# Kernel tuning notes

Measured on AMD Instinct MI355X. Metric: run time of the kernel, lower is better.

The kernel has to match this reference:

```python
import jax, jax.numpy as jnp
import numpy as np

B, S, E = 8, 2048, 8   # batch, seq, embed_dim (embed_dim forced to 8 by module structure)
NQ = 8                 # n_qubits
FF = 4096              # ffn_dim
LN_EPS = 1e-5


def setup_inputs() -> dict:
    key = jax.random.key(0)
    ks = jax.random.split(key, 16)
    rn = lambda k, shape, s=1.0: jax.random.normal(k, shape, dtype=jnp.float32) * s
    return {
        "x": rn(ks[0], (B, S, E)),
        "w_pre": rn(ks[1], (E, NQ), 0.3), "b_pre": rn(ks[2], (NQ,), 0.1),
        "th_q": rn(ks[3], (NQ,)), "th_k": rn(ks[4], (NQ,)), "th_v": rn(ks[5], (NQ,)),
        "w_comb": rn(ks[6], (E, E), 0.3), "b_comb": rn(ks[7], (E,), 0.1),
        "g1": jnp.ones((E,), jnp.float32), "be1": jnp.zeros((E,), jnp.float32),
        "g2": jnp.ones((E,), jnp.float32), "be2": jnp.zeros((E,), jnp.float32),
        "w_pre_f": rn(ks[8], (E, NQ), 0.3), "b_pre_f": rn(ks[9], (NQ,), 0.1),
        "th_f": rn(ks[10], (NQ,)),
        "w1": rn(ks[11], (NQ, FF), 0.3), "b1": rn(ks[12], (FF,), 0.1),
        "w2": rn(ks[13], (FF, E), 0.02), "b2": rn(ks[14], (E,), 0.1),
    }


def _qproj(z, theta):
    # Exact closed form of: RX(z_i)RX(theta_i) per wire on |0>, CNOT chain
    # (0,1)...(6,7),(7,0), then <Z_w>. CNOTs permute basis states; for the
    # resulting product distribution: <Z_k> = prod_{i<=k} cos(phi_i) (k>=1),
    # <Z_0> = prod_{i=1..NQ-1} cos(phi_i), with phi = z + theta.
    c = jnp.cos(z + theta)                 # [N, NQ]
    cp = jnp.cumprod(c, axis=-1)           # out_k for k>=1
    out0 = jnp.prod(c[..., 1:], axis=-1)   # wire 0
    return cp.at[..., 0].set(out0)


def _layernorm(z, g, b):
    m = jnp.mean(z, axis=-1, keepdims=True)
    v = jnp.var(z, axis=-1, keepdims=True)
    return (z - m) * jax.lax.rsqrt(v + LN_EPS) * g + b


def reference(x, w_pre, b_pre, th_q, th_k, th_v, w_comb, b_comb,
              g1, be1, g2, be2, w_pre_f, b_pre_f, th_f, w1, b1, w2, b2):
    b, s, e = x.shape
    xf = x.reshape(b * s, e)
    qin = xf @ w_pre + b_pre                       # shared pre_proj for q/k/v
    Q = _qproj(qin, th_q).reshape(b, s, e)         # num_heads=1, d_k=e=8
    K = _qproj(qin, th_k).reshape(b, s, e)
    V = _qproj(qin, th_v).reshape(b, s, e)
    scores = jnp.einsum('bqd,bkd->bqk', Q, K) / jnp.sqrt(jnp.float32(e))
    probs = jax.nn.softmax(scores, axis=-1)        # dropout=0 (eval)
    attn = jnp.einsum('bqk,bkd->bqd', probs, V)
    attn_out = attn @ w_comb + b_comb
    h = _layernorm(x + attn_out, g1, be1)
    hf = h.reshape(b * s, e)
    qf = _qproj(hf @ w_pre_f + b_pre_f, th_f)
    ff = jax.nn.relu(qf @ w1 + b1) @ w2 + b2
    return _layernorm(h + ff.reshape(b, s, e), g2, be2)
```

## Files before the change

kernel.cpp:

```cpp
#include <hip/hip_runtime.h>
#include <hip/hip_bf16.h>

#define BB 8
#define SS 2048
#define EE 8
#define FF 4096
#define NTOK (BB*SS)

using bf16x8 = __attribute__((ext_vector_type(8))) short;
using f32x4  = __attribute__((ext_vector_type(4))) float;

constexpr int O_FLAG  = 0;
constexpr int O_WPRE  = 8;
constexpr int O_BPRE  = 72;
constexpr int O_THQ   = 80;
constexpr int O_THK   = 88;
constexpr int O_THV   = 96;
constexpr int O_WCOMB = 104;
constexpr int O_BCOMB = 168;
constexpr int O_G1    = 176;
constexpr int O_BE1   = 184;
constexpr int O_G2    = 192;
constexpr int O_BE2   = 200;
constexpr int O_WPREF = 208;
constexpr int O_BPREF = 272;
constexpr int O_THF   = 280;
constexpr int O_B2    = 288;
constexpr int O_W1T   = 512;
constexpr int O_B1F   = O_W1T + FF*8;
constexpr int O_W2F   = O_B1F + FF;
constexpr int O_X     = O_W2F + FF*8;
constexpr int O_K     = O_X + NTOK*EE;
constexpr int O_V     = O_K + NTOK*EE;
constexpr int O_H     = O_V + NTOK*EE;
constexpr int O_P     = O_H + NTOK*EE;
constexpr int O_QFB   = O_P + 8*NTOK*EE;
constexpr int O_W1A   = O_QFB + NTOK*4;
constexpr int O_W2B   = O_W1A + 65536;
constexpr int O_QB    = O_W2B + 32768;
constexpr int O_KB    = O_QB + NTOK*4;
constexpr int O_VTB   = O_KB + NTOK*4;
constexpr size_t WS_MFMA = (size_t)(O_VTB + 65536) * 4;

__device__ __forceinline__ float b2f(unsigned short u) {
  return __uint_as_float(((unsigned)u) << 16);
}

__device__ __forceinline__ unsigned short f2bf(float f) {
  unsigned u = __float_as_uint(f);
  unsigned r = (u + 0x7fffu + ((u >> 16) & 1u)) >> 16;
  return (unsigned short)r;
}

__device__ __forceinline__ unsigned pk2(float a, float b) {
  unsigned ua = __float_as_uint(a) + 0x8000u;
  unsigned ub = __float_as_uint(b) + 0x8000u;
  return __builtin_amdgcn_perm(ub, ua, 0x07060302u);
}

__device__ __forceinline__ float loadin(const void* p, int i, int isf) {
  if (isf) return reinterpret_cast<const float*>(p)[i];
  return b2f(reinterpret_cast<const unsigned short*>(p)[i]);
}

__device__ __forceinline__ int detect_f32_wave(const void* x) {
  unsigned u = reinterpret_cast<const unsigned*>(x)[threadIdx.x & 63];
  float v = b2f((unsigned short)u);
  int bad = !(fabsf(v) <= 1e4f);
  return __ballot(bad) != 0ull;
}

__device__ __forceinline__ void qproj(const float* qin, const float* th, float* out) {
  float c[8];
#pragma unroll
  for (int i = 0; i < 8; ++i) c[i] = __cosf(qin[i] + th[i]);
  float p = c[1];
#pragma unroll
  for (int i = 2; i < 8; ++i) p *= c[i];
  out[0] = p;
  float r = c[0];
#pragma unroll
  for (int i = 1; i < 8; ++i) { r *= c[i]; out[i] = r; }
}

__device__ __forceinline__ void layernorm8(const float* z, const float* g, const float* b, float* y) {
  float m = 0.f;
#pragma unroll
  for (int i = 0; i < 8; ++i) m += z[i];
  m *= 0.125f;
  float v = 0.f;
#pragma unroll
  for (int i = 0; i < 8; ++i) { float d = z[i] - m; v += d * d; }
  v *= 0.125f;
  float rs = rsqrtf(v + 1e-5f);
#pragma unroll
  for (int i = 0; i < 8; ++i) y[i] = (z[i] - m) * rs * g[i] + b[i];
}

__global__ __launch_bounds__(256) void prep_all(
    const void* x, const void* w_pre, const void* b_pre, const void* th_q,
    const void* th_k, const void* th_v, const void* w_comb, const void* b_comb,
    const void* g1, const void* be1, const void* g2, const void* be2,
    const void* w_pre_f, const void* b_pre_f, const void* th_f,
    const void* w1, const void* b1, const void* w2, const void* b2,
    float* __restrict__ ws, int mfma_ok) {
  const int bid = blockIdx.x, tid = threadIdx.x;
  const int isf = detect_f32_wave(x);
  if (bid < 64) {
    const int tok = bid * 256 + tid;
    float xv[8];
#pragma unroll
    for (int d = 0; d < 8; ++d) xv[d] = loadin(x, tok * 8 + d, isf);
    float4* xp = reinterpret_cast<float4*>(ws + O_X + tok * 8);
    xp[0] = make_float4(xv[0], xv[1], xv[2], xv[3]);
    xp[1] = make_float4(xv[4], xv[5], xv[6], xv[7]);
    float qin[8];
#pragma unroll
    for (int i = 0; i < 8; ++i) {
      float a = loadin(b_pre, i, isf);
#pragma unroll
      for (int d = 0; d < 8; ++d) a = fmaf(xv[d], loadin(w_pre, d * 8 + i, isf), a);
      qin[i] = a;
    }
    float thq[8], thk[8], thv[8];
#pragma unroll
    for (int i = 0; i < 8; ++i) {
      thq[i] = loadin(th_q, i, isf);
      thk[i] = loadin(th_k, i, isf);
      thv[i] = loadin(th_v, i, isf);
    }
    float qv[8], kv[8], vv[8];
    qproj(qin, thq, qv);
    qproj(qin, thk, kv);
    qproj(qin, thv, vv);
    if (mfma_ok) {
      const float sc = 0.510120927f;
      uint4 uq, uk;
      uq.x = (unsigned)f2bf(qv[0] * sc) | ((unsigned)f2bf(qv[1] * sc) << 16);
      uq.y = (unsigned)f2bf(qv[2] * sc) | ((unsigned)f2bf(qv[3] * sc) << 16);
      uq.z = (unsigned)f2bf(qv[4] * sc) | ((unsigned)f2bf(qv[5] * sc) << 16);
      uq.w = (unsigned)f2bf(qv[6] * sc) | ((unsigned)f2bf(qv[7] * sc) << 16);
      uk.x = (unsigned)f2bf(kv[0]) | ((unsigned)f2bf(kv[1]) << 16);
      uk.y = (unsigned)f2bf(kv[2]) | ((unsigned)f2bf(kv[3]) << 16);
      uk.z = (unsigned)f2bf(kv[4]) | ((unsigned)f2bf(kv[5]) << 16);
      uk.w = (unsigned)f2bf(kv[6]) | ((unsigned)f2bf(kv[7]) << 16);
      reinterpret_cast<uint4*>(ws + O_QB)[tok] = uq;
      reinterpret_cast<uint4*>(ws + O_KB)[tok] = uk;
      unsigned short* vtb = reinterpret_cast<unsigned short*>(ws + O_VTB);
#pragma unroll
      for (int i = 0; i < 8; ++i) vtb[i * NTOK + tok] = f2bf(vv[i]);
    } else {
      float4* kp = reinterpret_cast<float4*>(ws + O_K + tok * 8);
      float4* vp = reinterpret_cast<float4*>(ws + O_V + tok * 8);
      kp[0] = make_float4(kv[0], kv[1], kv[2], kv[3]);
      kp[1] = make_float4(kv[4], kv[5], kv[6], kv[7]);
      vp[0] = make_float4(vv[0], vv[1], vv[2], vv[3]);
      vp[1] = make_float4(vv[4], vv[5], vv[6], vv[7]);
    }
  } else if (bid < 128) {
    if (!mfma_ok) return;
    const int idx = (bid - 64) * 256 + tid;
    const int T = idx >> 6, l = idx & 63, c = l & 15, g = l >> 4;
    const int j = T * 16 + c;
    float f[8];
#pragma unroll
    for (int e = 0; e < 8; ++e) f[e] = 0.f;
    if (g == 0) {
#pragma unroll
      for (int e = 0; e < 8; ++e) f[e] = loadin(w1, e * FF + j, isf);
    } else if (g == 1) {
      f[0] = loadin(b1, j, isf);
    }
    uint4 u;
    u.x = (unsigned)f2bf(f[0]) | ((unsigned)f2bf(f[1]) << 16);
    u.y = (unsigned)f2bf(f[2]) | ((unsigned)f2bf(f[3]) << 16);
    u.z = (unsigned)f2bf(f[4]) | ((unsigned)f2bf(f[5]) << 16);
    u.w = (unsigned)f2bf(f[6]) | ((unsigned)f2bf(f[7]) << 16);
    reinterpret_cast<uint4*>(ws + O_W1A)[idx] = u;
  } else if (bid < 160) {
    if (!mfma_ok) return;
    const int idx2 = (bid - 128) * 256 + tid;
    const int W = idx2 >> 6, l = idx2 & 63, i = l & 15, g = l >> 4;
    float f[8];
#pragma unroll
    for (int e = 0; e < 8; ++e) f[e] = 0.f;
    if (i < 8) {
#pragma unroll
      for (int e = 0; e < 8; ++e) {
        const int j = W * 32 + 16 * (e >> 2) + 4 * g + (e & 3);
        f[e] = loadin(w2, j * 8 + i, isf);
      }
    }
    uint4 u;
    u.x = (unsigned)f2bf(f[0]) | ((unsigned)f2bf(f[1]) << 16);
    u.y = (unsigned)f2bf(f[2]) | ((unsigned)f2bf(f[3]) << 16);
    u.z = (unsigned)f2bf(f[4]) | ((unsigned)f2bf(f[5]) << 16);
    u.w = (unsigned)f2bf(f[6]) | ((unsigned)f2bf(f[7]) << 16);
    reinterpret_cast<uint4*>(ws + O_W2B)[idx2] = u;
  } else if (bid == 160) {
    if (tid < 64) {
      ws[O_WPRE + tid]  = loadin(w_pre, tid, isf);
      ws[O_WCOMB + tid] = loadin(w_comb, tid, isf);
      ws[O_WPREF + tid] = loadin(w_pre_f, tid, isf);
    }
    if (tid < 8) {
      ws[O_BPRE + tid]  = loadin(b_pre, tid, isf);
      ws[O_THQ + tid]   = loadin(th_q, tid, isf);
      ws[O_THK + tid]   = loadin(th_k, tid, isf);
      ws[O_THV + tid]   = loadin(th_v, tid, isf);
      ws[O_BCOMB + tid] = loadin(b_comb, tid, isf);
      ws[O_G1 + tid]    = loadin(g1, tid, isf);
      ws[O_BE1 + tid]   = loadin(be1, tid, isf);
      ws[O_G2 + tid]    = loadin(g2, tid, isf);
      ws[O_BE2 + tid]   = loadin(be2, tid, isf);
      ws[O_BPREF + tid] = loadin(b_pre_f, tid, isf);
      ws[O_THF + tid]   = loadin(th_f, tid, isf);
      ws[O_B2 + tid]    = loadin(b2, tid, isf);
    }
    if (tid == 0) ws[O_FLAG] = (float)isf;
  } else {
    if (mfma_ok) return;
    const int j = (bid - 161) * 256 + tid;
    ws[O_B1F + j] = loadin(b1, j, isf);
#pragma unroll
    for (int i = 0; i < 8; ++i) {
      ws[O_W1T + j * 8 + i] = loadin(w1, i * FF + j, isf);
      ws[O_W2F + j * 8 + i] = loadin(w2, j * 8 + i, isf);
    }
  }
}

__global__ __launch_bounds__(256) void attn_mfma(const float* __restrict__ ws,
                                                 float* __restrict__ hout,
                                                 unsigned* __restrict__ qfb_out) {
  __shared__ float Olds[4][32][8];
  __shared__ float Llds[4 * 32];
  const int tid = threadIdx.x;
  const int wv = tid >> 6, l = tid & 63;
  const int c = l & 15, g = l >> 4;
  const int batch = blockIdx.x >> 6;
  const int qbase = blockIdx.x * 32;

  const bf16x8 zerov = (bf16x8)(short)0;
  const f32x4 zero = {0.f, 0.f, 0.f, 0.f};

  bf16x8 qb0 = zerov, qb1 = zerov;
  if (g == 0) {
    qb0 = reinterpret_cast<const bf16x8*>(ws + O_QB)[qbase + c];
    qb1 = reinterpret_cast<const bf16x8*>(ws + O_QB)[qbase + 16 + c];
  }

  const bf16x8* Kb = reinterpret_cast<const bf16x8*>(ws + O_KB);
  const unsigned short* vtb = reinterpret_cast<const unsigned short*>(ws + O_VTB);

  f32x4 oacc0 = zero, oacc1 = zero;
  float lsum0 = 0.f, lsum1 = 0.f;
  const int kbase = batch * SS + wv * 512;

  for (int w = 0; w < 16; ++w) {
    const int kt = kbase + w * 32;
    bf16x8 kf0 = zerov, kf1 = zerov;
    if (g == 0) {
      kf0 = Kb[kt + c];
      kf1 = Kb[kt + 16 + c];
    }
    f32x4 s0 = __builtin_amdgcn_mfma_f32_16x16x32_bf16(kf0, qb0, zero, 0, 0, 0);
    f32x4 s1 = __builtin_amdgcn_mfma_f32_16x16x32_bf16(kf1, qb0, zero, 0, 0, 0);
    f32x4 s2 = __builtin_amdgcn_mfma_f32_16x16x32_bf16(kf0, qb1, zero, 0, 0, 0);
    f32x4 s3 = __builtin_amdgcn_mfma_f32_16x16x32_bf16(kf1, qb1, zero, 0, 0, 0);
    float p0[4], p1[4], p2[4], p3[4];
#pragma unroll
    for (int r = 0; r < 4; ++r) {
      p0[r] = __builtin_amdgcn_exp2f(s0[r]);
      p1[r] = __builtin_amdgcn_exp2f(s1[r]);
      p2[r] = __builtin_amdgcn_exp2f(s2[r]);
      p3[r] = __builtin_amdgcn_exp2f(s3[r]);
      lsum0 += p0[r] + p1[r];
      lsum1 += p2[r] + p3[r];
    }
    union { unsigned u[4]; bf16x8 v; } PA0, PA1;
    PA0.u[0] = pk2(p0[0], p0[1]);
    PA0.u[1] = pk2(p0[2], p0[3]);
    PA0.u[2] = pk2(p1[0], p1[1]);
    PA0.u[3] = pk2(p1[2], p1[3]);
    PA1.u[0] = pk2(p2[0], p2[1]);
    PA1.u[1] = pk2(p2[2], p2[3]);
    PA1.u[2] = pk2(p3[0], p3[1]);
    PA1.u[3] = pk2(p3[2], p3[3]);
    union { uint2 u[2]; bf16x8 v; } VF;
    VF.u[0] = make_uint2(0u, 0u);
    VF.u[1] = make_uint2(0u, 0u);
    if (c < 8) {
      VF.u[0] = *reinterpret_cast<const uint2*>(vtb + c * NTOK + kt + 4 * g);
      VF.u[1] = *reinterpret_cast<const uint2*>(vtb + c * NTOK + kt + 16 + 4 * g);
    }
    oacc0 = __builtin_amdgcn_mfma_f32_16x16x32_bf16(PA0.v, VF.v, oacc0, 0, 0, 0);
    oacc1 = __builtin_amdgcn_mfma_f32_16x16x32_bf16(PA1.v, VF.v, oacc1, 0, 0, 0);
  }

  lsum0 += __shfl_xor(lsum0, 16);
  lsum0 += __shfl_xor(lsum0, 32);
  lsum1 += __shfl_xor(lsum1, 16);
  lsum1 += __shfl_xor(lsum1, 32);
  if (l < 16) {
    Llds[wv * 32 + l] = lsum0;
    Llds[wv * 32 + 16 + l] = lsum1;
  }
  if (c < 8) {
#pragma unroll
    for (int r = 0; r < 4; ++r) {
      Olds[wv][4 * g + r][c] = oacc0[r];
      Olds[wv][16 + 4 * g + r][c] = oacc1[r];
    }
  }
  __syncthreads();

  if (tid < 32) {
    const int mytok = qbase + tid;
    float lv = Llds[tid] + Llds[32 + tid] + Llds[64 + tid] + Llds[96 + tid];
    const float inv = 1.0f / lv;
    float o[8];
#pragma unroll
    for (int i = 0; i < 8; ++i)
      o[i] = (Olds[0][tid][i] + Olds[1][tid][i] + Olds[2][tid][i] + Olds[3][tid][i]) * inv;
    float at[8];
#pragma unroll
    for (int i = 0; i < 8; ++i) {
      float a = ws[O_BCOMB + i];
#pragma unroll
      for (int d = 0; d < 8; ++d) a = fmaf(o[d], ws[O_WCOMB + d * 8 + i], a);
      at[i] = a;
    }
    const float* xp = ws + O_X + mytok * 8;
    float z[8];
#pragma unroll
    for (int i = 0; i < 8; ++i) z[i] = xp[i] + at[i];
    float y[8];
    layernorm8(z, ws + O_G1, ws + O_BE1, y);
    float4* hp = reinterpret_cast<float4*>(hout + mytok * 8);
    hp[0] = make_float4(y[0], y[1], y[2], y[3]);
    hp[1] = make_float4(y[4], y[5], y[6], y[7]);
    float qin2[8];
#pragma unroll
    for (int i = 0; i < 8; ++i) {
      float a = ws[O_BPREF + i];
#pragma unroll
      for (int d = 0; d < 8; ++d) a = fmaf(y[d], ws[O_WPREF + d * 8 + i], a);
      qin2[i] = a;
    }
    float qfv[8];
    qproj(qin2, ws + O_THF, qfv);
    uint4 u;
    u.x = (unsigned)f2bf(qfv[0]) | ((unsigned)f2bf(qfv[1]) << 16);
    u.y = (unsigned)f2bf(qfv[2]) | ((unsigned)f2bf(qfv[3]) << 16);
    u.z = (unsigned)f2bf(qfv[4]) | ((unsigned)f2bf(qfv[5]) << 16);
    u.w = (unsigned)f2bf(qfv[6]) | ((unsigned)f2bf(qfv[7]) << 16);
    reinterpret_cast<uint4*>(qfb_out)[mytok] = u;
  }
}

__global__ __launch_bounds__(512) void ffn_mfma_ln2(const float* __restrict__ ws,
                                                    void* __restrict__ out) {
  __shared__ float Olds[8][64][8];
  const int tid = threadIdx.x;
  const int wv = tid >> 6, l = tid & 63;
  const int c = l & 15, g = l >> 4;
  const int tokbase = blockIdx.x * 64;

  bf16x8 qfb0 = (bf16x8)(short)0, qfb1 = qfb0, qfb2 = qfb0, qfb3 = qfb0;
  if (g == 0) {
    const bf16x8* qp = reinterpret_cast<const bf16x8*>(ws + O_QFB) + tokbase + c;
    qfb0 = qp[0]; qfb1 = qp[16]; qfb2 = qp[32]; qfb3 = qp[48];
  } else if (g == 1) {
    qfb0[0] = (short)0x3F80; qfb1[0] = (short)0x3F80;
    qfb2[0] = (short)0x3F80; qfb3[0] = (short)0x3F80;
  }

  const bf16x8* w1a = reinterpret_cast<const bf16x8*>(ws + O_W1A) + l;
  const bf16x8* w2b = reinterpret_cast<const bf16x8*>(ws + O_W2B) + l;
  const f32x4 zero = {0.f, 0.f, 0.f, 0.f};
  f32x4 acc0 = zero, acc1 = zero, acc2 = zero, acc3 = zero;

  bf16x8 W10 = w1a[(wv * 32 + 0) * 64], W11 = w1a[(wv * 32 + 1) * 64];
  bf16x8 W12 = w1a[(wv * 32 + 2) * 64], W13 = w1a[(wv * 32 + 3) * 64];
  bf16x8 W20 = w2b[(wv * 16 + 0) * 64], W21 = w2b[(wv * 16 + 1) * 64];

  for (int jt = 0; jt < 8; ++jt) {
    bf16x8 nW10, nW11, nW12, nW13, nW20, nW21;
    if (jt < 7) {
      const int Tb = wv * 32 + (jt + 1) * 4;
      const int Wb = wv * 16 + (jt + 1) * 2;
      nW10 = w1a[(Tb + 0) * 64]; nW11 = w1a[(Tb + 1) * 64];
      nW12 = w1a[(Tb + 2) * 64]; nW13 = w1a[(Tb + 3) * 64];
      nW20 = w2b[(Wb + 0) * 64]; nW21 = w2b[(Wb + 1) * 64];
    }
#define FFN_TOK(QF, ACC)                                                        \
    {                                                                           \
      f32x4 p0 = __builtin_amdgcn_mfma_f32_16x16x32_bf16(W10, QF, zero, 0,0,0); \
      f32x4 p1 = __builtin_amdgcn_mfma_f32_16x16x32_bf16(W11, QF, zero, 0,0,0); \
      f32x4 p2 = __builtin_amdgcn_mfma_f32_16x16x32_bf16(W12, QF, zero, 0,0,0); \
      f32x4 p3 = __builtin_amdgcn_mfma_f32_16x16x32_bf16(W13, QF, zero, 0,0,0); \
      union { unsigned u[4]; bf16x8 v; } A0, A1;                                \
      A0.u[0] = pk2(fmaxf(p0[0], 0.f), fmaxf(p0[1], 0.f));                      \
      A0.u[1] = pk2(fmaxf(p0[2], 0.f), fmaxf(p0[3], 0.f));                      \
      A0.u[2] = pk2(fmaxf(p1[0], 0.f), fmaxf(p1[1], 0.f));                      \
      A0.u[3] = pk2(fmaxf(p1[2], 0.f), fmaxf(p1[3], 0.f));                      \
      A1.u[0] = pk2(fmaxf(p2[0], 0.f), fmaxf(p2[1], 0.f));                      \
      A1.u[1] = pk2(fmaxf(p2[2], 0.f), fmaxf(p2[3], 0.f));                      \
      A1.u[2] = pk2(fmaxf(p3[0], 0.f), fmaxf(p3[1], 0.f));                      \
      A1.u[3] = pk2(fmaxf(p3[2], 0.f), fmaxf(p3[3], 0.f));                      \
      ACC = __builtin_amdgcn_mfma_f32_16x16x32_bf16(A0.v, W20, ACC, 0, 0, 0);   \
      ACC = __builtin_amdgcn_mfma_f32_16x16x32_bf16(A1.v, W21, ACC, 0, 0, 0);   \
    }
    FFN_TOK(qfb0, acc0)
    FFN_TOK(qfb1, acc1)
    FFN_TOK(qfb2, acc2)
    FFN_TOK(qfb3, acc3)
#undef FFN_TOK
    if (jt < 7) {
      W10 = nW10; W11 = nW11; W12 = nW12; W13 = nW13;
      W20 = nW20; W21 = nW21;
    }
  }

  if (c < 8) {
#pragma unroll
    for (int r = 0; r < 4; ++r) {
      Olds[wv][ 0 + 4 * g + r][c] = acc0[r];
      Olds[wv][16 + 4 * g + r][c] = acc1[r];
      Olds[wv][32 + 4 * g + r][c] = acc2[r];
      Olds[wv][48 + 4 * g + r][c] = acc3[r];
    }
  }
  __syncthreads();

  if (tid < 64) {
    const int tok = tokbase + tid;
    const int isf = (int)ws[O_FLAG];
    float f[8];
#pragma unroll
    for (int d = 0; d < 8; ++d) {
      float s = ws[O_B2 + d];
#pragma unroll
      for (int w = 0; w < 8; ++w) s += Olds[w][tid][d];
      f[d] = s;
    }
    const float* hp = ws + O_H + tok * 8;
    float z[8];
#pragma unroll
    for (int d = 0; d < 8; ++d) z[d] = hp[d] + f[d];
    float y[8];
    layernorm8(z, ws + O_G2, ws + O_BE2, y);
    if (isf) {
      float4* op = reinterpret_cast<float4*>((float*)out + tok * 8);
      op[0] = make_float4(y[0], y[1], y[2], y[3]);
      op[1] = make_float4(y[4], y[5], y[6], y[7]);
    } else {
      uint4 o;
      o.x = (unsigned)f2bf(y[0]) | ((unsigned)f2bf(y[1]) << 16);
      o.y = (unsigned)f2bf(y[2]) | ((unsigned)f2bf(y[3]) << 16);
      o.z = (unsigned)f2bf(y[4]) | ((unsigned)f2bf(y[5]) << 16);
      o.w = (unsigned)f2bf(y[6]) | ((unsigned)f2bf(y[7]) << 16);
      *reinterpret_cast<uint4*>((unsigned short*)out + tok * 8) = o;
    }
  }
}

__global__ __launch_bounds__(256) void attn_ln1(const float* __restrict__ ws,
                                                float* __restrict__ hout) {
  __shared__ float Kt[512 * 8];
  __shared__ float Vt[512 * 8];
  __shared__ float plds[8 * 32 * 9];
  const int tid = threadIdx.x;
  const int batch = blockIdx.x >> 6;
  const int chunk = blockIdx.x & 63;
  const int qlocal = tid & 31;
  const int part = tid >> 5;
  const int tok = batch * SS + chunk * 32 + qlocal;

  float qs[8];
  {
    const float* xp = ws + O_X + tok * 8;
    float qin[8];
#pragma unroll
    for (int i = 0; i < 8; ++i) {
      float a = ws[O_BPRE + i];
#pragma unroll
      for (int d = 0; d < 8; ++d) a = fmaf(xp[d], ws[O_WPRE + d * 8 + i], a);
      qin[i] = a;
    }
    float qv[8];
    qproj(qin, ws + O_THQ, qv);
#pragma unroll
    for (int i = 0; i < 8; ++i) qs[i] = qv[i] * 0.510120927f;
  }

  float ll = 0.f;
  float acc[8];
#pragma unroll
  for (int i = 0; i < 8; ++i) acc[i] = 0.f;

  for (int t = 0; t < 4; ++t) {
    const float4* Kg = reinterpret_cast<const float4*>(ws + O_K + (batch * SS + t * 512) * 8);
    const float4* Vg = reinterpret_cast<const float4*>(ws + O_V + (batch * SS + t * 512) * 8);
    float4* Kt4 = reinterpret_cast<float4*>(Kt);
    float4* Vt4 = reinterpret_cast<float4*>(Vt);
#pragma unroll
    for (int i = 0; i < 4; ++i) {
      Kt4[i * 256 + tid] = Kg[i * 256 + tid];
      Vt4[i * 256 + tid] = Vg[i * 256 + tid];
    }
    __syncthreads();
    const float* Kp = Kt + part * 64 * 8;
    const float* Vp = Vt + part * 64 * 8;
#pragma unroll 2
    for (int k = 0; k < 64; ++k) {
      float4 ka = *reinterpret_cast<const float4*>(Kp + k * 8);
      float4 kb = *reinterpret_cast<const float4*>(Kp + k * 8 + 4);
      float s = ((qs[0] * ka.x + qs[1] * ka.y) + (qs[2] * ka.z + qs[3] * ka.w)) +
                ((qs[4] * kb.x + qs[5] * kb.y) + (qs[6] * kb.z + qs[7] * kb.w));
      float p = __builtin_amdgcn_exp2f(s);
      ll += p;
      float4 va = *reinterpret_cast<const float4*>(Vp + k * 8);
      float4 vb = *reinterpret_cast<const float4*>(Vp + k * 8 + 4);
      acc[0] = fmaf(p, va.x, acc[0]);
      acc[1] = fmaf(p, va.y, acc[1]);
      acc[2] = fmaf(p, va.z, acc[2]);
      acc[3] = fmaf(p, va.w, acc[3]);
      acc[4] = fmaf(p, vb.x, acc[4]);
      acc[5] = fmaf(p, vb.y, acc[5]);
      acc[6] = fmaf(p, vb.z, acc[6]);
      acc[7] = fmaf(p, vb.w, acc[7]);
    }
    __syncthreads();
  }

  float* pp = plds + (part * 32 + qlocal) * 9;
#pragma unroll
  for (int i = 0; i < 8; ++i) pp[i] = acc[i];
  pp[8] = ll;
  __syncthreads();

  if (tid < 32) {
    float o[8];
    float ls = 0.f;
#pragma unroll
    for (int i = 0; i < 8; ++i) o[i] = 0.f;
#pragma unroll
    for (int pr = 0; pr < 8; ++pr) {
      const float* q = plds + (pr * 32 + tid) * 9;
#pragma unroll
      for (int i = 0; i < 8; ++i) o[i] += q[i];
      ls += q[8];
    }
    const float inv = 1.0f / ls;
#pragma unroll
    for (int i = 0; i < 8; ++i) o[i] *= inv;
    const int mytok = batch * SS + chunk * 32 + tid;
    float at[8];
#pragma unroll
    for (int i = 0; i < 8; ++i) {
      float a = ws[O_BCOMB + i];
#pragma unroll
      for (int d = 0; d < 8; ++d) a = fmaf(o[d], ws[O_WCOMB + d * 8 + i], a);
      at[i] = a;
    }
    const float* xp = ws + O_X + mytok * 8;
    float z[8];
#pragma unroll
    for (int i = 0; i < 8; ++i) z[i] = xp[i] + at[i];
    float y[8];
    layernorm8(z, ws + O_G1, ws + O_BE1, y);
    float4* hp = reinterpret_cast<float4*>(hout + mytok * 8);
    hp[0] = make_float4(y[0], y[1], y[2], y[3]);
    hp[1] = make_float4(y[4], y[5], y[6], y[7]);
  }
}

__global__ __launch_bounds__(256) void ffn_ln2(const float* __restrict__ ws,
                                               void* __restrict__ out) {
  __shared__ float plds[4 * 64 * 8];
  const int tid = threadIdx.x;
  const int tok = blockIdx.x * 64 + (tid & 63);
  const int part = __builtin_amdgcn_readfirstlane(tid >> 6);

  const float* hp = ws + O_H + tok * 8;
  float4 h0 = *reinterpret_cast<const float4*>(hp);
  float4 h1 = *reinterpret_cast<const float4*>(hp + 4);
  float hv[8] = {h0.x, h0.y, h0.z, h0.w, h1.x, h1.y, h1.z, h1.w};

  float qin[8];
#pragma unroll
  for (int i = 0; i < 8; ++i) {
    float a = ws[O_BPREF + i];
#pragma unroll
    for (int d = 0; d < 8; ++d) a = fmaf(hv[d], ws[O_WPREF + d * 8 + i], a);
    qin[i] = a;
  }
  float qf[8];
  qproj(qin, ws + O_THF, qf);

  float acc[8];
#pragma unroll
  for (int i = 0; i < 8; ++i) acc[i] = 0.f;
  const float* w1t = ws + O_W1T + part * 1024 * 8;
  const float* b1f = ws + O_B1F + part * 1024;
  const float* w2f = ws + O_W2F + part * 1024 * 8;
#pragma unroll 4
  for (int j = 0; j < 1024; ++j) {
    float hj = b1f[j];
    const float* wa = w1t + j * 8;
#pragma unroll
    for (int d = 0; d < 8; ++d) hj = fmaf(qf[d], wa[d], hj);
    hj = fmaxf(hj, 0.f);
    const float* wb = w2f + j * 8;
#pragma unroll
    for (int d = 0; d < 8; ++d) acc[d] = fmaf(hj, wb[d], acc[d]);
  }

  float* pp = plds + part * 512 + (tid & 63) * 8;
#pragma unroll
  for (int d = 0; d < 8; ++d) pp[d] = acc[d];
  __syncthreads();

  if (tid < 64) {
    const int isf = (int)ws[O_FLAG];
    float f[8];
#pragma unroll
    for (int d = 0; d < 8; ++d)
      f[d] = ws[O_B2 + d] + plds[tid * 8 + d] + plds[512 + tid * 8 + d] +
             plds[1024 + tid * 8 + d] + plds[1536 + tid * 8 + d];
    float z[8];
#pragma unroll
    for (int d = 0; d < 8; ++d) z[d] = hv[d] + f[d];
    float y[8];
    layernorm8(z, ws + O_G2, ws + O_BE2, y);
    const int otok = blockIdx.x * 64 + tid;
    if (isf) {
      float4* op = reinterpret_cast<float4*>((float*)out + otok * 8);
      op[0] = make_float4(y[0], y[1], y[2], y[3]);
      op[1] = make_float4(y[4], y[5], y[6], y[7]);
    } else {
      uint4 o;
      o.x = (unsigned)f2bf(y[0]) | ((unsigned)f2bf(y[1]) << 16);
      o.y = (unsigned)f2bf(y[2]) | ((unsigned)f2bf(y[3]) << 16);
      o.z = (unsigned)f2bf(y[4]) | ((unsigned)f2bf(y[5]) << 16);
      o.w = (unsigned)f2bf(y[6]) | ((unsigned)f2bf(y[7]) << 16);
      *reinterpret_cast<uint4*>((unsigned short*)out + otok * 8) = o;
    }
  }
}

extern "C" void kernel_launch(void* const* d_in, const int* in_sizes, int n_in,
                              void* d_out, int out_size, void* d_ws, size_t ws_size,
                              hipStream_t stream) {
  float* ws = (float*)d_ws;
  const int mfma_ok = (ws_size >= WS_MFMA);

  prep_all<<<dim3(177), dim3(256), 0, stream>>>(
      d_in[0], d_in[1], d_in[2], d_in[3], d_in[4], d_in[5], d_in[6], d_in[7],
      d_in[8], d_in[9], d_in[10], d_in[11], d_in[12], d_in[13], d_in[14],
      d_in[15], d_in[16], d_in[17], d_in[18], ws, mfma_ok);

  if (mfma_ok) {
    attn_mfma<<<dim3(512), dim3(256), 0, stream>>>(ws, ws + O_H,
                                                   (unsigned*)(ws + O_QFB));
    ffn_mfma_ln2<<<dim3(256), dim3(512), 0, stream>>>(ws, d_out);
  } else {
    attn_ln1<<<dim3(512), dim3(256), 0, stream>>>(ws, ws + O_H);
    ffn_ln2<<<dim3(256), dim3(256), 0, stream>>>(ws, d_out);
  }
}
```

Baseline: 35.93 us.

## Fuse attention and FFN into one 512-thread kernel with LDS handoff

Merges the attention+LN1 kernel and the FFN+LN2 kernel into a single kernel. Each block handles 64 tokens across 8 waves, and the LN1 output and FFN input are kept in shared memory instead of round-tripping through the workspace. x is read directly from the input with vectorized loads rather than a copied workspace buffer. This removes a launch and global traffic, at the cost of lower attention parallelism (256 blocks instead of 512) and a device-function split with an entry wrapper.

```diff
diff --git a/kernel.cpp b/kernel.cpp
--- a/kernel.cpp
+++ b/kernel.cpp
@@ -63,6 +63,21 @@
   return b2f(reinterpret_cast<const unsigned short*>(p)[i]);
 }
 
+__device__ __forceinline__ void loadx8(const void* x, int tok, int isf, float* xv) {
+  if (isf) {
+    float4 a = reinterpret_cast<const float4*>(x)[tok * 2];
+    float4 b = reinterpret_cast<const float4*>(x)[tok * 2 + 1];
+    xv[0] = a.x; xv[1] = a.y; xv[2] = a.z; xv[3] = a.w;
+    xv[4] = b.x; xv[5] = b.y; xv[6] = b.z; xv[7] = b.w;
+  } else {
+    uint4 u = reinterpret_cast<const uint4*>(x)[tok];
+    xv[0] = __uint_as_float(u.x << 16); xv[1] = __uint_as_float(u.x & 0xffff0000u);
+    xv[2] = __uint_as_float(u.y << 16); xv[3] = __uint_as_float(u.y & 0xffff0000u);
+    xv[4] = __uint_as_float(u.z << 16); xv[5] = __uint_as_float(u.z & 0xffff0000u);
+    xv[6] = __uint_as_float(u.w << 16); xv[7] = __uint_as_float(u.w & 0xffff0000u);
+  }
+}
+
 __device__ __forceinline__ int detect_f32_wave(const void* x) {
   unsigned u = reinterpret_cast<const unsigned*>(x)[threadIdx.x & 63];
   float v = b2f((unsigned short)u);
@@ -109,11 +124,7 @@
   if (bid < 64) {
     const int tok = bid * 256 + tid;
     float xv[8];
-#pragma unroll
-    for (int d = 0; d < 8; ++d) xv[d] = loadin(x, tok * 8 + d, isf);
-    float4* xp = reinterpret_cast<float4*>(ws + O_X + tok * 8);
-    xp[0] = make_float4(xv[0], xv[1], xv[2], xv[3]);
-    xp[1] = make_float4(xv[4], xv[5], xv[6], xv[7]);
+    loadx8(x, tok, isf, xv);
     float qin[8];
 #pragma unroll
     for (int i = 0; i < 8; ++i) {
@@ -150,6 +161,9 @@
 #pragma unroll
       for (int i = 0; i < 8; ++i) vtb[i * NTOK + tok] = f2bf(vv[i]);
     } else {
+      float4* xp = reinterpret_cast<float4*>(ws + O_X + tok * 8);
+      xp[0] = make_float4(xv[0], xv[1], xv[2], xv[3]);
+      xp[1] = make_float4(xv[4], xv[5], xv[6], xv[7]);
       float4* kp = reinterpret_cast<float4*>(ws + O_K + tok * 8);
       float4* vp = reinterpret_cast<float4*>(ws + O_V + tok * 8);
       kp[0] = make_float4(kv[0], kv[1], kv[2], kv[3]);
@@ -230,63 +244,42 @@
   }
 }
 
-__global__ __launch_bounds__(256) void attn_mfma(const float* __restrict__ ws,
-                                                 float* __restrict__ hout,
-                                                 unsigned* __restrict__ qfb_out) {
-  __shared__ float Olds[4][32][8];
-  __shared__ float Llds[4 * 32];
+__global__ __launch_bounds__(512) void attn_ffn_fused(const void* __restrict__ x,
+                                                      const float* __restrict__ ws,
+                                                      void* __restrict__ out,
+                                                      int isf) {
+  __shared__ float Olds[8][64][8];
+  __shared__ float Llds[8][64];
+  __shared__ float Hlds[64][8];
+  __shared__ unsigned Qflds[64 * 4];
   const int tid = threadIdx.x;
   const int wv = tid >> 6, l = tid & 63;
   const int c = l & 15, g = l >> 4;
-  const int batch = blockIdx.x >> 6;
-  const int qbase = blockIdx.x * 32;
+  const int tokbase = blockIdx.x * 64;
+  const int batch = blockIdx.x >> 5;
 
   const bf16x8 zerov = (bf16x8)(short)0;
   const f32x4 zero = {0.f, 0.f, 0.f, 0.f};
 
-  bf16x8 qb0 = zerov, qb1 = zerov;
+  bf16x8 qb0 = zerov, qb1 = zerov, qb2 = zerov, qb3 = zerov;
   if (g == 0) {
-    qb0 = reinterpret_cast<const bf16x8*>(ws + O_QB)[qbase + c];
-    qb1 = reinterpret_cast<const bf16x8*>(ws + O_QB)[qbase + 16 + c];
-  }
-
+    const bf16x8* qp = reinterpret_cast<const bf16x8*>(ws + O_QB) + tokbase + c;
+    qb0 = qp[0]; qb1 = qp[16]; qb2 = qp[32]; qb3 = qp[48];
+  }
   const bf16x8* Kb = reinterpret_cast<const bf16x8*>(ws + O_KB);
   const unsigned short* vtb = reinterpret_cast<const unsigned short*>(ws + O_VTB);
 
-  f32x4 oacc0 = zero, oacc1 = zero;
-  float lsum0 = 0.f, lsum1 = 0.f;
-  const int kbase = batch * SS + wv * 512;
-
-  for (int w = 0; w < 16; ++w) {
+  f32x4 oacc0 = zero, oacc1 = zero, oacc2 = zero, oacc3 = zero;
+  float ls0 = 0.f, ls1 = 0.f, ls2 = 0.f, ls3 = 0.f;
+  const int kbase = batch * SS + wv * 256;
+
+  for (int w = 0; w < 8; ++w) {
     const int kt = kbase + w * 32;
     bf16x8 kf0 = zerov, kf1 = zerov;
     if (g == 0) {
       kf0 = Kb[kt + c];
       kf1 = Kb[kt + 16 + c];
     }
-    f32x4 s0 = __builtin_amdgcn_mfma_f32_16x16x32_bf16(kf0, qb0, zero, 0, 0, 0);
-    f32x4 s1 = __builtin_amdgcn_mfma_f32_16x16x32_bf16(kf1, qb0, zero, 0, 0, 0);
-    f32x4 s2 = __builtin_amdgcn_mfma_f32_16x16x32_bf16(kf0, qb1, zero, 0, 0, 0);
-    f32x4 s3 = __builtin_amdgcn_mfma_f32_16x16x32_bf16(kf1, qb1, zero, 0, 0, 0);
-    float p0[4], p1[4], p2[4], p3[4];
-#pragma unroll
-    for (int r = 0; r < 4; ++r) {
-      p0[r] = __builtin_amdgcn_exp2f(s0[r]);
-      p1[r] = __builtin_amdgcn_exp2f(s1[r]);
-      p2[r] = __builtin_amdgcn_exp2f(s2[r]);
-      p3[r] = __builtin_amdgcn_exp2f(s3[r]);
-      lsum0 += p0[r] + p1[r];
-      lsum1 += p2[r] + p3[r];
-    }
-    union { unsigned u[4]; bf16x8 v; } PA0, PA1;
-    PA0.u[0] = pk2(p0[0], p0[1]);
-    PA0.u[1] = pk2(p0[2], p0[3]);
-    PA0.u[2] = pk2(p1[0], p1[1]);
-    PA0.u[3] = pk2(p1[2], p1[3]);
-    PA1.u[0] = pk2(p2[0], p2[1]);
-    PA1.u[1] = pk2(p2[2], p2[3]);
-    PA1.u[2] = pk2(p3[0], p3[1]);
-    PA1.u[3] = pk2(p3[2], p3[3]);
     union { uint2 u[2]; bf16x8 v; } VF;
     VF.u[0] = make_uint2(0u, 0u);
     VF.u[1] = make_uint2(0u, 0u);
@@ -294,35 +287,67 @@
       VF.u[0] = *reinterpret_cast<const uint2*>(vtb + c * NTOK + kt + 4 * g);
       VF.u[1] = *reinterpret_cast<const uint2*>(vtb + c * NTOK + kt + 16 + 4 * g);
     }
-    oacc0 = __builtin_amdgcn_mfma_f32_16x16x32_bf16(PA0.v, VF.v, oacc0, 0, 0, 0);
-    oacc1 = __builtin_amdgcn_mfma_f32_16x16x32_bf16(PA1.v, VF.v, oacc1, 0, 0, 0);
-  }
-
-  lsum0 += __shfl_xor(lsum0, 16);
-  lsum0 += __shfl_xor(lsum0, 32);
-  lsum1 += __shfl_xor(lsum1, 16);
-  lsum1 += __shfl_xor(lsum1, 32);
+#define ATT_QT(QB, OACC, LS)                                                     \
+    {                                                                            \
+      f32x4 s0 = __builtin_amdgcn_mfma_f32_16x16x32_bf16(kf0, QB, zero, 0,0,0);  \
+      f32x4 s1 = __builtin_amdgcn_mfma_f32_16x16x32_bf16(kf1, QB, zero, 0,0,0);  \
+      float p0[4], p1[4];                                                        \
+      _Pragma("unroll")                                                          \
+      for (int r = 0; r < 4; ++r) {                                              \
+        p0[r] = __builtin_amdgcn_exp2f(s0[r]);                                   \
+        p1[r] = __builtin_amdgcn_exp2f(s1[r]);                                   \
+        LS += p0[r] + p1[r];                                                     \
+      }                                                                          \
+      union { unsigned u[4]; bf16x8 v; } PA;                                     \
+      PA.u[0] = pk2(p0[0], p0[1]);                                               \
+      PA.u[1] = pk2(p0[2], p0[3]);                                               \
+      PA.u[2] = pk2(p1[0], p1[1]);                                               \
+      PA.u[3] = pk2(p1[2], p1[3]);                                               \
+      OACC = __builtin_amdgcn_mfma_f32_16x16x32_bf16(PA.v, VF.v, OACC, 0, 0, 0); \
+    }
+    ATT_QT(qb0, oacc0, ls0)
+    ATT_QT(qb1, oacc1, ls1)
+    ATT_QT(qb2, oacc2, ls2)
+    ATT_QT(qb3, oacc3, ls3)
+#undef ATT_QT
+  }
+
+  ls0 += __shfl_xor(ls0, 16); ls0 += __shfl_xor(ls0, 32);
+  ls1 += __shfl_xor(ls1, 16); ls1 += __shfl_xor(ls1, 32);
+  ls2 += __shfl_xor(ls2, 16); ls2 += __shfl_xor(ls2, 32);
+  ls3 += __shfl_xor(ls3, 16); ls3 += __shfl_xor(ls3, 32);
   if (l < 16) {
-    Llds[wv * 32 + l] = lsum0;
-    Llds[wv * 32 + 16 + l] = lsum1;
+    Llds[wv][l]      = ls0;
+    Llds[wv][16 + l] = ls1;
+    Llds[wv][32 + l] = ls2;
+    Llds[wv][48 + l] = ls3;
   }
   if (c < 8) {
 #pragma unroll
     for (int r = 0; r < 4; ++r) {
-      Olds[wv][4 * g + r][c] = oacc0[r];
+      Olds[wv][ 0 + 4 * g + r][c] = oacc0[r];
       Olds[wv][16 + 4 * g + r][c] = oacc1[r];
+      Olds[wv][32 + 4 * g + r][c] = oacc2[r];
+      Olds[wv][48 + 4 * g + r][c] = oacc3[r];
     }
   }
   __syncthreads();
 
-  if (tid < 32) {
-    const int mytok = qbase + tid;
-    float lv = Llds[tid] + Llds[32 + tid] + Llds[64 + tid] + Llds[96 + tid];
+  if (tid < 64) {
+    const int mytok = tokbase + tid;
+    float lv = 0.f;
+    float o[8];
+#pragma unroll
+    for (int i = 0; i < 8; ++i) o[i] = 0.f;
+#pragma unroll
+    for (int w = 0; w < 8; ++w) {
+      lv += Llds[w][tid];
+#pragma unroll
+      for (int i = 0; i < 8; ++i) o[i] += Olds[w][tid][i];
+    }
     const float inv = 1.0f / lv;
-    float o[8];
-#pragma unroll
-    for (int i = 0; i < 8; ++i)
-      o[i] = (Olds[0][tid][i] + Olds[1][tid][i] + Olds[2][tid][i] + Olds[3][tid][i]) * inv;
+#pragma unroll
+    for (int i = 0; i < 8; ++i) o[i] *= inv;
     float at[8];
 #pragma unroll
     for (int i = 0; i < 8; ++i) {
@@ -331,15 +356,15 @@
       for (int d = 0; d < 8; ++d) a = fmaf(o[d], ws[O_WCOMB + d * 8 + i], a);
       at[i] = a;
     }
-    const float* xp = ws + O_X + mytok * 8;
+    float xv[8];
+    loadx8(x, mytok, isf, xv);
     float z[8];
 #pragma unroll
-    for (int i = 0; i < 8; ++i) z[i] = xp[i] + at[i];
+    for (int i = 0; i < 8; ++i) z[i] = xv[i] + at[i];
     float y[8];
     layernorm8(z, ws + O_G1, ws + O_BE1, y);
-    float4* hp = reinterpret_cast<float4*>(hout + mytok * 8);
-    hp[0] = make_float4(y[0], y[1], y[2], y[3]);
-    hp[1] = make_float4(y[4], y[5], y[6], y[7]);
+#pragma unroll
+    for (int i = 0; i < 8; ++i) Hlds[tid][i] = y[i];
     float qin2[8];
 #pragma unroll
     for (int i = 0; i < 8; ++i) {
@@ -350,26 +375,16 @@
     }
     float qfv[8];
     qproj(qin2, ws + O_THF, qfv);
-    uint4 u;
-    u.x = (unsigned)f2bf(qfv[0]) | ((unsigned)f2bf(qfv[1]) << 16);
-    u.y = (unsigned)f2bf(qfv[2]) | ((unsigned)f2bf(qfv[3]) << 16);
-    u.z = (unsigned)f2bf(qfv[4]) | ((unsigned)f2bf(qfv[5]) << 16);
-    u.w = (unsigned)f2bf(qfv[6]) | ((unsigned)f2bf(qfv[7]) << 16);
-    reinterpret_cast<uint4*>(qfb_out)[mytok] = u;
-  }
-}
-
-__global__ __launch_bounds__(512) void ffn_mfma_ln2(const float* __restrict__ ws,
-                                                    void* __restrict__ out) {
-  __shared__ float Olds[8][64][8];
-  const int tid = threadIdx.x;
-  const int wv = tid >> 6, l = tid & 63;
-  const int c = l & 15, g = l >> 4;
-  const int tokbase = blockIdx.x * 64;
+    Qflds[tid * 4 + 0] = (unsigned)f2bf(qfv[0]) | ((unsigned)f2bf(qfv[1]) << 16);
+    Qflds[tid * 4 + 1] = (unsigned)f2bf(qfv[2]) | ((unsigned)f2bf(qfv[3]) << 16);
+    Qflds[tid * 4 + 2] = (unsigned)f2bf(qfv[4]) | ((unsigned)f2bf(qfv[5]) << 16);
+    Qflds[tid * 4 + 3] = (unsigned)f2bf(qfv[6]) | ((unsigned)f2bf(qfv[7]) << 16);
+  }
+  __syncthreads();
 
   bf16x8 qfb0 = (bf16x8)(short)0, qfb1 = qfb0, qfb2 = qfb0, qfb3 = qfb0;
   if (g == 0) {
-    const bf16x8* qp = reinterpret_cast<const bf16x8*>(ws + O_QFB) + tokbase + c;
+    const bf16x8* qp = reinterpret_cast<const bf16x8*>(Qflds) + c;
     qfb0 = qp[0]; qfb1 = qp[16]; qfb2 = qp[32]; qfb3 = qp[48];
   } else if (g == 1) {
     qfb0[0] = (short)0x3F80; qfb1[0] = (short)0x3F80;
@@ -378,7 +393,6 @@
 
   const bf16x8* w1a = reinterpret_cast<const bf16x8*>(ws + O_W1A) + l;
   const bf16x8* w2b = reinterpret_cast<const bf16x8*>(ws + O_W2B) + l;
-  const f32x4 zero = {0.f, 0.f, 0.f, 0.f};
   f32x4 acc0 = zero, acc1 = zero, acc2 = zero, acc3 = zero;
 
   bf16x8 W10 = w1a[(wv * 32 + 0) * 64], W11 = w1a[(wv * 32 + 1) * 64];
@@ -436,7 +450,6 @@
 
   if (tid < 64) {
     const int tok = tokbase + tid;
-    const int isf = (int)ws[O_FLAG];
     float f[8];
 #pragma unroll
     for (int d = 0; d < 8; ++d) {
@@ -445,10 +458,9 @@
       for (int w = 0; w < 8; ++w) s += Olds[w][tid][d];
       f[d] = s;
     }
-    const float* hp = ws + O_H + tok * 8;
     float z[8];
 #pragma unroll
-    for (int d = 0; d < 8; ++d) z[d] = hp[d] + f[d];
+    for (int d = 0; d < 8; ++d) z[d] = Hlds[tid][d] + f[d];
     float y[8];
     layernorm8(z, ws + O_G2, ws + O_BE2, y);
     if (isf) {
@@ -465,6 +477,7 @@
     }
   }
 }
+
 
 __global__ __launch_bounds__(256) void attn_ln1(const float* __restrict__ ws,
                                                 float* __restrict__ hout) {
@@ -651,6 +664,10 @@
   }
 }
 
+__global__ __launch_bounds__(512) void attn_ffn_entry(const void* __restrict__ x,
+                                                      const float* __restrict__ ws,
+                                                      void* __restrict__ out);
+
 extern "C" void kernel_launch(void* const* d_in, const int* in_sizes, int n_in,
                               void* d_out, int out_size, void* d_ws, size_t ws_size,
                               hipStream_t stream) {
@@ -663,11 +680,250 @@
       d_in[15], d_in[16], d_in[17], d_in[18], ws, mfma_ok);
 
   if (mfma_ok) {
-    attn_mfma<<<dim3(512), dim3(256), 0, stream>>>(ws, ws + O_H,
-                                                   (unsigned*)(ws + O_QFB));
-    ffn_mfma_ln2<<<dim3(256), dim3(512), 0, stream>>>(ws, d_out);
+    attn_ffn_entry<<<dim3(256), dim3(512), 0, stream>>>(d_in[0], ws, d_out);
   } else {
     attn_ln1<<<dim3(512), dim3(256), 0, stream>>>(ws, ws + O_H);
     ffn_ln2<<<dim3(256), dim3(256), 0, stream>>>(ws, d_out);
   }
 }
+
+__global__ __launch_bounds__(512) void attn_ffn_entry(const void* __restrict__ x,
+                                                      const float* __restrict__ ws,
+                                                      void* __restrict__ out) {
+  const int isf = detect_f32_wave(x);
+  extern __device__ void attn_ffn_body(const void*, const float*, void*, int);
+  attn_ffn_body(x, ws, out, isf);
+}
+
+__device__ void attn_ffn_body(const void* __restrict__ x,
+                              const float* __restrict__ ws,
+                              void* __restrict__ out, int isf) {
+  __shared__ float Olds[8][64][8];
+  __shared__ float Llds[8][64];
+  __shared__ float Hlds[64][8];
+  __shared__ unsigned Qflds[64 * 4];
+  const int tid = threadIdx.x;
+  const int wv = tid >> 6, l = tid & 63;
+  const int c = l & 15, g = l >> 4;
+  const int tokbase = blockIdx.x * 64;
+  const int batch = blockIdx.x >> 5;
+
+  const bf16x8 zerov = (bf16x8)(short)0;
+  const f32x4 zero = {0.f, 0.f, 0.f, 0.f};
+
+  bf16x8 qb0 = zerov, qb1 = zerov, qb2 = zerov, qb3 = zerov;
+  if (g == 0) {
+    const bf16x8* qp = reinterpret_cast<const bf16x8*>(ws + O_QB) + tokbase + c;
+    qb0 = qp[0]; qb1 = qp[16]; qb2 = qp[32]; qb3 = qp[48];
+  }
+  const bf16x8* Kb = reinterpret_cast<const bf16x8*>(ws + O_KB);
+  const unsigned short* vtb = reinterpret_cast<const unsigned short*>(ws + O_VTB);
+
+  f32x4 oacc0 = zero, oacc1 = zero, oacc2 = zero, oacc3 = zero;
+  float ls0 = 0.f, ls1 = 0.f, ls2 = 0.f, ls3 = 0.f;
+  const int kbase = batch * SS + wv * 256;
+
+  for (int w = 0; w < 8; ++w) {
+    const int kt = kbase + w * 32;
+    bf16x8 kf0 = zerov, kf1 = zerov;
+    if (g == 0) {
+      kf0 = Kb[kt + c];
+      kf1 = Kb[kt + 16 + c];
+    }
+    union { uint2 u[2]; bf16x8 v; } VF;
+    VF.u[0] = make_uint2(0u, 0u);
+    VF.u[1] = make_uint2(0u, 0u);
+    if (c < 8) {
+      VF.u[0] = *reinterpret_cast<const uint2*>(vtb + c * NTOK + kt + 4 * g);
+      VF.u[1] = *reinterpret_cast<const uint2*>(vtb + c * NTOK + kt + 16 + 4 * g);
+    }
+#define ATT_QT(QB, OACC, LS)                                                     \
+    {                                                                            \
+      f32x4 s0 = __builtin_amdgcn_mfma_f32_16x16x32_bf16(kf0, QB, zero, 0,0,0);  \
+      f32x4 s1 = __builtin_amdgcn_mfma_f32_16x16x32_bf16(kf1, QB, zero, 0,0,0);  \
+      float p0[4], p1[4];                                                        \
+      _Pragma("unroll")                                                          \
+      for (int r = 0; r < 4; ++r) {                                              \
+        p0[r] = __builtin_amdgcn_exp2f(s0[r]);                                   \
+        p1[r] = __builtin_amdgcn_exp2f(s1[r]);                                   \
+        LS += p0[r] + p1[r];                                                     \
+      }                                                                          \
+      union { unsigned u[4]; bf16x8 v; } PA;                                     \
+      PA.u[0] = pk2(p0[0], p0[1]);                                               \
+      PA.u[1] = pk2(p0[2], p0[3]);                                               \
+      PA.u[2] = pk2(p1[0], p1[1]);                                               \
+      PA.u[3] = pk2(p1[2], p1[3]);                                               \
+      OACC = __builtin_amdgcn_mfma_f32_16x16x32_bf16(PA.v, VF.v, OACC, 0, 0, 0); \
+    }
+    ATT_QT(qb0, oacc0, ls0)
+    ATT_QT(qb1, oacc1, ls1)
+    ATT_QT(qb2, oacc2, ls2)
+    ATT_QT(qb3, oacc3, ls3)
+#undef ATT_QT
+  }
+
+  ls0 += __shfl_xor(ls0, 16); ls0 += __shfl_xor(ls0, 32);
+  ls1 += __shfl_xor(ls1, 16); ls1 += __shfl_xor(ls1, 32);
+  ls2 += __shfl_xor(ls2, 16); ls2 += __shfl_xor(ls2, 32);
+  ls3 += __shfl_xor(ls3, 16); ls3 += __shfl_xor(ls3, 32);
+  if (l < 16) {
+    Llds[wv][l]      = ls0;
+    Llds[wv][16 + l] = ls1;
+    Llds[wv][32 + l] = ls2;
+    Llds[wv][48 + l] = ls3;
+  }
+  if (c < 8) {
+#pragma unroll
+    for (int r = 0; r < 4; ++r) {
+      Olds[wv][ 0 + 4 * g + r][c] = oacc0[r];
+      Olds[wv][16 + 4 * g + r][c] = oacc1[r];
+      Olds[wv][32 + 4 * g + r][c] = oacc2[r];
+      Olds[wv][48 + 4 * g + r][c] = oacc3[r];
+    }
+  }
+  __syncthreads();
+
+  if (tid < 64) {
+    const int mytok = tokbase + tid;
+    float lv = 0.f;
+    float o[8];
+#pragma unroll
+    for (int i = 0; i < 8; ++i) o[i] = 0.f;
+#pragma unroll
+    for (int w = 0; w < 8; ++w) {
+      lv += Llds[w][tid];
+#pragma unroll
+      for (int i = 0; i < 8; ++i) o[i] += Olds[w][tid][i];
+    }
+    const float inv = 1.0f / lv;
+#pragma unroll
+    for (int i = 0; i < 8; ++i) o[i] *= inv;
+    float at[8];
+#pragma unroll
+    for (int i = 0; i < 8; ++i) {
+      float a = ws[O_BCOMB + i];
+#pragma unroll
+      for (int d = 0; d < 8; ++d) a = fmaf(o[d], ws[O_WCOMB + d * 8 + i], a);
+      at[i] = a;
+    }
+    float xv[8];
+    loadx8(x, mytok, isf, xv);
+    float z[8];
+#pragma unroll
+    for (int i = 0; i < 8; ++i) z[i] = xv[i] + at[i];
+    float y[8];
+    layernorm8(z, ws + O_G1, ws + O_BE1, y);
+#pragma unroll
+    for (int i = 0; i < 8; ++i) Hlds[tid][i] = y[i];
+    float qin2[8];
+#pragma unroll
+    for (int i = 0; i < 8; ++i) {
+      float a = ws[O_BPREF + i];
+#pragma unroll
+      for (int d = 0; d < 8; ++d) a = fmaf(y[d], ws[O_WPREF + d * 8 + i], a);
+      qin2[i] = a;
+    }
+    float qfv[8];
+    qproj(qin2, ws + O_THF, qfv);
+    Qflds[tid * 4 + 0] = (unsigned)f2bf(qfv[0]) | ((unsigned)f2bf(qfv[1]) << 16);
+    Qflds[tid * 4 + 1] = (unsigned)f2bf(qfv[2]) | ((unsigned)f2bf(qfv[3]) << 16);
+    Qflds[tid * 4 + 2] = (unsigned)f2bf(qfv[4]) | ((unsigned)f2bf(qfv[5]) << 16);
+    Qflds[tid * 4 + 3] = (unsigned)f2bf(qfv[6]) | ((unsigned)f2bf(qfv[7]) << 16);
+  }
+  __syncthreads();
+
+  bf16x8 qfb0 = (bf16x8)(short)0, qfb1 = qfb0, qfb2 = qfb0, qfb3 = qfb0;
+  if (g == 0) {
+    const bf16x8* qp = reinterpret_cast<const bf16x8*>(Qflds) + c;
+    qfb0 = qp[0]; qfb1 = qp[16]; qfb2 = qp[32]; qfb3 = qp[48];
+  } else if (g == 1) {
+    qfb0[0] = (short)0x3F80; qfb1[0] = (short)0x3F80;
+    qfb2[0] = (short)0x3F80; qfb3[0] = (short)0x3F80;
+  }
+
+  const bf16x8* w1a = reinterpret_cast<const bf16x8*>(ws + O_W1A) + l;
+  const bf16x8* w2b = reinterpret_cast<const bf16x8*>(ws + O_W2B) + l;
+  f32x4 acc0 = zero, acc1 = zero, acc2 = zero, acc3 = zero;
+
+  bf16x8 W10 = w1a[(wv * 32 + 0) * 64], W11 = w1a[(wv * 32 + 1) * 64];
+  bf16x8 W12 = w1a[(wv * 32 + 2) * 64], W13 = w1a[(wv * 32 + 3) * 64];
+  bf16x8 W20 = w2b[(wv * 16 + 0) * 64], W21 = w2b[(wv * 16 + 1) * 64];
+
+  for (int jt = 0; jt < 8; ++jt) {
+    bf16x8 nW10, nW11, nW12, nW13, nW20, nW21;
+    if (jt < 7) {
+      const int Tb = wv * 32 + (jt + 1) * 4;
+      const int Wb = wv * 16 + (jt + 1) * 2;
+      nW10 = w1a[(Tb + 0) * 64]; nW11 = w1a[(Tb + 1) * 64];
+      nW12 = w1a[(Tb + 2) * 64]; nW13 = w1a[(Tb + 3) * 64];
+      nW20 = w2b[(Wb + 0) * 64]; nW21 = w2b[(Wb + 1) * 64];
+    }
+#define FFN_TOK(QF, ACC)                                                        \
+    {                                                                           \
+      f32x4 p0 = __builtin_amdgcn_mfma_f32_16x16x32_bf16(W10, QF, zero, 0,0,0); \
+      f32x4 p1 = __builtin_amdgcn_mfma_f32_16x16x32_bf16(W11, QF, zero, 0,0,0); \
+      f32x4 p2 = __builtin_amdgcn_mfma_f32_16x16x32_bf16(W12, QF, zero, 0,0,0); \
+      f32x4 p3 = __builtin_amdgcn_mfma_f32_16x16x32_bf16(W13, QF, zero, 0,0,0); \
+      union { unsigned u[4]; bf16x8 v; } A0, A1;                                \
+      A0.u[0] = pk2(fmaxf(p0[0], 0.f), fmaxf(p0[1], 0.f));                      \
+      A0.u[1] = pk2(fmaxf(p0[2], 0.f), fmaxf(p0[3], 0.f));                      \
+      A0.u[2] = pk2(fmaxf(p1[0], 0.f), fmaxf(p1[1], 0.f));                      \
+      A0.u[3] = pk2(fmaxf(p1[2], 0.f), fmaxf(p1[3], 0.f));                      \
+      A1.u[0] = pk2(fmaxf(p2[0], 0.f), fmaxf(p2[1], 0.f));                      \
+      A1.u[1] = pk2(fmaxf(p2[2], 0.f), fmaxf(p2[3], 0.f));                      \
+      A1.u[2] = pk2(fmaxf(p3[0], 0.f), fmaxf(p3[1], 0.f));                      \
+      A1.u[3] = pk2(fmaxf(p3[2], 0.f), fmaxf(p3[3], 0.f));                      \
+      ACC = __builtin_amdgcn_mfma_f32_16x16x32_bf16(A0.v, W20, ACC, 0, 0, 0);   \
+      ACC = __builtin_amdgcn_mfma_f32_16x16x32_bf16(A1.v, W21, ACC, 0, 0, 0);   \
+    }
+    FFN_TOK(qfb0, acc0)
+    FFN_TOK(qfb1, acc1)
+    FFN_TOK(qfb2, acc2)
+    FFN_TOK(qfb3, acc3)
+#undef FFN_TOK
+    if (jt < 7) {
+      W10 = nW10; W11 = nW11; W12 = nW12; W13 = nW13;
+      W20 = nW20; W21 = nW21;
+    }
+  }
+
+  if (c < 8) {
+#pragma unroll
+    for (int r = 0; r < 4; ++r) {
+      Olds[wv][ 0 + 4 * g + r][c] = acc0[r];
+      Olds[wv][16 + 4 * g + r][c] = acc1[r];
+      Olds[wv][32 + 4 * g + r][c] = acc2[r];
+      Olds[wv][48 + 4 * g + r][c] = acc3[r];
+    }
+  }
+  __syncthreads();
+
+  if (tid < 64) {
+    const int tok = tokbase + tid;
+    float f[8];
+#pragma unroll
+    for (int d = 0; d < 8; ++d) {
+      float s = ws[O_B2 + d];
+#pragma unroll
+      for (int w = 0; w < 8; ++w) s += Olds[w][tid][d];
+      f[d] = s;
+    }
+    float z[8];
+#pragma unroll
+    for (int d = 0; d < 8; ++d) z[d] = Hlds[tid][d] + f[d];
+    float y[8];
+    layernorm8(z, ws + O_G2, ws + O_BE2, y);
+    if (isf) {
+      float4* op = reinterpret_cast<float4*>((float*)out + tok * 8);
+      op[0] = make_float4(y[0], y[1], y[2], y[3]);
+      op[1] = make_float4(y[4], y[5], y[6], y[7]);
+    } else {
+      uint4 o;
+      o.x = (unsigned)f2bf(y[0]) | ((unsigned)f2bf(y[1]) << 16);
+      o.y = (unsigned)f2bf(y[2]) | ((unsigned)f2bf(y[3]) << 16);
+      o.z = (unsigned)f2bf(y[4]) | ((unsigned)f2bf(y[5]) << 16);
+      o.w = (unsigned)f2bf(y[6]) | ((unsigned)f2bf(y[7]) << 16);
+      *reinterpret_cast<uint4*>((unsigned short*)out + tok * 8) = o;
+    }
+  }
+}
```

Measured after the change: 30.61 us. 14.8% less time.
